# Optimization experiments

Hardware: AMD Instinct MI355X
Metric: run time of the kernel (lower is better)

Reference implementation:

```python
import jax, jax.numpy as jnp
import numpy as np

B, T, D, H = 4, 2048, 1024, 16
HD = D // H  # 64
EPS = 1e-5

def _layernorm(x, g, b):
    mu = jnp.mean(x, axis=-1, keepdims=True)
    var = jnp.var(x, axis=-1, keepdims=True)
    return (x - mu) * jax.lax.rsqrt(var + EPS) * g + b

def setup_inputs() -> dict:
    key = jax.random.key(0)
    ks = jax.random.split(key, 8)
    s = D ** -0.5
    return {
        "x":  jax.random.normal(ks[0], (B, T, D), jnp.float32),
        "Wq": jax.random.normal(ks[1], (H, D, HD), jnp.float32) * s,
        "Wk": jax.random.normal(ks[2], (H, D, HD), jnp.float32) * s,
        "Wv": jax.random.normal(ks[3], (H, D, HD), jnp.float32) * s,
        "Wp": jax.random.normal(ks[4], (D, D), jnp.float32) * s,
        "bp": jnp.zeros((D,), jnp.float32),
        "W1": jax.random.normal(ks[5], (D, 4 * D), jnp.float32) * s,
        "b1": jnp.zeros((4 * D,), jnp.float32),
        "W2": jax.random.normal(ks[6], (4 * D, D), jnp.float32) * (4 * D) ** -0.5,
        "b2": jnp.zeros((D,), jnp.float32),
        "g1": jnp.ones((D,), jnp.float32),
        "be1": jnp.zeros((D,), jnp.float32),
        "g2": jnp.ones((D,), jnp.float32),
        "be2": jnp.zeros((D,), jnp.float32),
    }

def reference(x, Wq, Wk, Wv, Wp, bp, W1, b1, W2, b2, g1, be1, g2, be2):
    # --- pre-LN causal MHA (all heads batched; torch code loops per head) ---
    h = _layernorm(x, g1, be1)                       # [B,T,D]
    q = jnp.einsum('btd,hdk->bhtk', h, Wq)
    k = jnp.einsum('btd,hdk->bhtk', h, Wk)
    v = jnp.einsum('btd,hdk->bhtk', h, Wv)
    scores = jnp.einsum('bhtk,bhsk->bhts', q, k) * (HD ** -0.5)
    causal = jnp.tril(jnp.ones((T, T), bool))
    scores = jnp.where(causal, scores, -jnp.inf)
    w = jax.nn.softmax(scores, axis=-1)              # [B,H,T,T]
    o = jnp.einsum('bhts,bhsk->bhtk', w, v)          # [B,H,T,HD]
    o = o.transpose(0, 2, 1, 3).reshape(x.shape[0], x.shape[1], D)  # concat heads
    x = x + o @ Wp + bp                              # residual 1
    # --- pre-LN FFN ---
    h2 = _layernorm(x, g2, be2)
    ff = jax.nn.relu(h2 @ W1 + b1) @ W2 + b2
    return x + ff
```

## Files before the change

kernel.cpp:

```cpp
#include <hip/hip_runtime.h>
#include <hip/hip_bf16.h>
#include <math.h>

#define Bsz 4
#define Tsz 2048
#define Dsz 1024
#define Hn  16
#define HDs 64

typedef __attribute__((ext_vector_type(8))) short bf16x8;
typedef __attribute__((ext_vector_type(4))) float f32x4;

typedef const __attribute__((address_space(1))) void gvoid;
typedef __attribute__((address_space(3))) void lvoid;

__device__ __forceinline__ void async_copy16(const short* g, short* l) {
    __builtin_amdgcn_global_load_lds((gvoid*)g, (lvoid*)l, 16, 0, 0);
}

__device__ __forceinline__ short f2bf(float x) {
    __hip_bfloat16 h = __float2bfloat16(x);
    return *reinterpret_cast<short*>(&h);
}

__device__ __forceinline__ unsigned int pack_bf16(float hi, float lo) {
    unsigned int uh = __float_as_uint(hi) + 0x8000u;
    unsigned int ul = __float_as_uint(lo) + 0x8000u;
    return __builtin_amdgcn_perm(uh, ul, 0x07060302u);
}

__device__ __forceinline__ size_t headed_idx(int m, int c) {
    int b = m >> 11, t = m & 2047, h = c >> 6, kc = c & 63;
    return (((size_t)(b * Hn + h) * Tsz + t) << 6) + kc;
}

__global__ __launch_bounds__(256) void ln_kernel(const float* __restrict__ x,
                                                 const float* __restrict__ g,
                                                 const float* __restrict__ beta,
                                                 short* __restrict__ out)
{
    const int row = blockIdx.x;
    const float* xr = x + (size_t)row * Dsz;
    float v[4];
    float s = 0.f, s2 = 0.f;
#pragma unroll
    for (int i = 0; i < 4; ++i) {
        v[i] = xr[threadIdx.x + 256 * i];
        s += v[i];
        s2 += v[i] * v[i];
    }
#pragma unroll
    for (int off = 32; off; off >>= 1) {
        s  += __shfl_xor(s,  off);
        s2 += __shfl_xor(s2, off);
    }
    __shared__ float red[8];
    const int wave = threadIdx.x >> 6;
    if ((threadIdx.x & 63) == 0) { red[wave * 2] = s; red[wave * 2 + 1] = s2; }
    __syncthreads();
    s  = red[0] + red[2] + red[4] + red[6];
    s2 = red[1] + red[3] + red[5] + red[7];
    const float mu  = s * (1.f / Dsz);
    const float var = s2 * (1.f / Dsz) - mu * mu;
    const float rs  = rsqrtf(var + 1e-5f);
    short* orow = out + (size_t)row * Dsz;
#pragma unroll
    for (int i = 0; i < 4; ++i) {
        int col = threadIdx.x + 256 * i;
        orow[col] = f2bf((v[i] - mu) * rs * g[col] + beta[col]);
    }
}

__global__ __launch_bounds__(256) void transpose_cvt(
    const float* __restrict__ in, short* __restrict__ outp, int R, int C)
{
    __shared__ float tile[32][33];
    const int r0 = blockIdx.y * 32, c0 = blockIdx.x * 32;
    const size_t so = (size_t)blockIdx.z * R * C;
    const int tx = threadIdx.x & 31, ty = threadIdx.x >> 5;
    const float* ip = in + so;
    short* op = outp + so;
#pragma unroll
    for (int i = 0; i < 4; ++i)
        tile[ty + i * 8][tx] = ip[(size_t)(r0 + ty + i * 8) * C + c0 + tx];
    __syncthreads();
#pragma unroll
    for (int i = 0; i < 4; ++i)
        op[(size_t)(c0 + ty + i * 8) * R + r0 + tx] = f2bf(tile[tx][ty + i * 8]);
}

__global__ __launch_bounds__(256) void transpose_cvt_qkv(
    const float* __restrict__ Wq, const float* __restrict__ Wk,
    const float* __restrict__ Wv, short* __restrict__ outp)
{
    __shared__ float tile[32][33];
    const int z = blockIdx.z;
    const float* in = (z < 16) ? Wq : (z < 32) ? Wk : Wv;
    const int zz = z & 15;
    const int r0 = blockIdx.y * 32, c0 = blockIdx.x * 32;
    const int tx = threadIdx.x & 31, ty = threadIdx.x >> 5;
    const float* ip = in + (size_t)zz * (1024 * 64);
    short* op = outp + (size_t)z * (1024 * 64);
#pragma unroll
    for (int i = 0; i < 4; ++i)
        tile[ty + i * 8][tx] = ip[(size_t)(r0 + ty + i * 8) * 64 + c0 + tx];
    __syncthreads();
#pragma unroll
    for (int i = 0; i < 4; ++i)
        op[(size_t)(c0 + ty + i * 8) * 1024 + r0 + tx] = f2bf(tile[tx][ty + i * 8]);
}

template <int EPI>
__global__ __launch_bounds__(256) void gemm_mfma(
    const short* __restrict__ A, const short* __restrict__ Bt,
    const float* __restrict__ bias, const float* __restrict__ resid,
    float* __restrict__ Cf, short* __restrict__ Cb0,
    short* __restrict__ Cb1, short* __restrict__ Cb2,
    int M, int N, int K, float scale)
{
    __shared__ short As[128 * 32];
    __shared__ short Bs[128 * 32];
    const int tid  = threadIdx.x;
    const int lane = tid & 63, wave = tid >> 6;
    const int quad = lane >> 4, l16 = lane & 15;
    const int m0 = blockIdx.y * 128, n0 = blockIdx.x * 128;
    const int wm = (wave >> 1) * 64, wn = (wave & 1) * 64;

    f32x4 acc[4][4];
#pragma unroll
    for (int i = 0; i < 4; ++i)
#pragma unroll
        for (int j = 0; j < 4; ++j) acc[i][j] = f32x4{0.f, 0.f, 0.f, 0.f};

    const short* gA = A  + (size_t)(m0 + wave * 32 + (lane >> 2)) * K + (lane & 3) * 8;
    const short* gB = Bt + (size_t)(n0 + wave * 32 + (lane >> 2)) * K + (lane & 3) * 8;
    short* lA0 = As + wave * 1024;
    short* lA1 = As + wave * 1024 + 512;
    short* lB0 = Bs + wave * 1024;
    short* lB1 = Bs + wave * 1024 + 512;
    const size_t rstep = (size_t)16 * K;

    for (int k0 = 0; k0 < K; k0 += 32) {
        async_copy16(gA,         lA0);
        async_copy16(gA + rstep, lA1);
        async_copy16(gB,         lB0);
        async_copy16(gB + rstep, lB1);
        gA += 32; gB += 32;
        __syncthreads();
        bf16x8 af[4], bfr[4];
#pragma unroll
        for (int mt = 0; mt < 4; ++mt)
            af[mt] = *(const bf16x8*)(As + (wm + mt * 16 + l16) * 32 + quad * 8);
#pragma unroll
        for (int nt = 0; nt < 4; ++nt)
            bfr[nt] = *(const bf16x8*)(Bs + (wn + nt * 16 + l16) * 32 + quad * 8);
#pragma unroll
        for (int mt = 0; mt < 4; ++mt)
#pragma unroll
            for (int nt = 0; nt < 4; ++nt)
                acc[mt][nt] = __builtin_amdgcn_mfma_f32_16x16x32_bf16(
                    af[mt], bfr[nt], acc[mt][nt], 0, 0, 0);
        __syncthreads();
    }

#pragma unroll
    for (int mt = 0; mt < 4; ++mt) {
#pragma unroll
        for (int nt = 0; nt < 4; ++nt) {
#pragma unroll
            for (int r = 0; r < 4; ++r) {
                const int m = m0 + wm + mt * 16 + quad * 4 + r;
                const int c = n0 + wn + nt * 16 + l16;
                float val = acc[mt][nt][r];
                if (EPI == 0) {
                    const int sel = c >> 10, cl = c & 1023;
                    if (sel == 0)
                        Cb0[headed_idx(m, cl)] = f2bf(val * scale);
                    else if (sel == 1)
                        Cb1[headed_idx(m, cl)] = f2bf(val);
                    else {
                        int b = m >> 11, t = m & 2047;
                        size_t idx = ((((size_t)((b << 4) | (cl >> 6)) << 6) | (cl & 63)) << 11) | t;
                        Cb2[idx] = f2bf(val);
                    }
                } else if (EPI == 2) {
                    size_t idx = (size_t)m * N + c;
                    Cf[idx] = val + bias[c] + resid[idx];
                } else {
                    float v2 = val + bias[c];
                    Cb0[(size_t)m * N + c] = f2bf(v2 > 0.f ? v2 : 0.f);
                }
            }
        }
    }
}

__global__ __launch_bounds__(256, 3) void fattn_kernel(
    const short* __restrict__ Q,
    const short* __restrict__ K,
    const short* __restrict__ VT,
    short* __restrict__ O)
{
    __shared__ short Kl[2][64 * 64];
    __shared__ short Vl[2][64 * 64];
    __shared__ short p_lds[4][2][16 * 64];
    const int tid  = threadIdx.x;
    const int lane = tid & 63, wave = tid >> 6;
    const int quad = lane >> 4, l16 = lane & 15;

    const int tile = 15 - blockIdx.x;
    const int q0   = tile * 128;
    const int q0w  = q0 + wave * 32;
    const int bh   = blockIdx.y;
    const int bb = bh >> 4, hh = bh & 15;
    const size_t bhoff = (size_t)bh * (Tsz * HDs);
    const short* Qb = Q + bhoff;
    const short* Kb = K + bhoff;
    const short* Vb = VT + bhoff;

    const int s_a = tid, s_b = tid + 256;
    const int ra = s_a >> 3, ga = (s_a & 7) ^ (ra & 7);
    const int rb = s_b >> 3, gb = (s_b & 7) ^ (rb & 7);

    short* pw[2] = { &p_lds[wave][0][0], &p_lds[wave][1][0] };
    const int rd0 = l16 * 64 + (((quad    ) ^ (l16 & 7)) << 3);
    const int rd1 = l16 * 64 + (((quad + 4) ^ (l16 & 7)) << 3);

    bf16x8 bq[2][2];
#pragma unroll
    for (int mt = 0; mt < 2; ++mt) {
        const short* qp = Qb + (size_t)(q0w + mt * 16 + l16) * 64 + quad * 8;
        bq[mt][0] = *(const bf16x8*)qp;
        bq[mt][1] = *(const bf16x8*)(qp + 32);
    }

    f32x4 oaccT[2][4];
    float lacc[2] = {0.f, 0.f};
#pragma unroll
    for (int mt = 0; mt < 2; ++mt)
#pragma unroll
        for (int nt = 0; nt < 4; ++nt) oaccT[mt][nt] = f32x4{0.f, 0.f, 0.f, 0.f};

    const int nch  = (q0 + 127) / 64 + 1;
    const int cmax = (q0w + 31) / 64;

    auto stage = [&](int c, int buf) {
        const int c64 = c * 64;
        short* kb_l = &Kl[buf][0];
        short* vb_l = &Vl[buf][0];
        async_copy16(Kb + (((size_t)(c64 + ra)) << 6) + (ga << 3), kb_l + s_a * 8);
        async_copy16(Kb + (((size_t)(c64 + rb)) << 6) + (gb << 3), kb_l + s_b * 8);
        async_copy16(Vb + ((size_t)ra << 11) + c64 + (ga << 3), vb_l + s_a * 8);
        async_copy16(Vb + ((size_t)rb << 11) + c64 + (gb << 3), vb_l + s_b * 8);
    };

    stage(0, 0);
    __syncthreads();

    for (int c = 0; c < nch; ++c) {
        const int cur = c & 1;
        if (c + 1 < nch) stage(c + 1, cur ^ 1);

        if (c <= cmax) {
            const int s0 = c * 64;
            const short* Kc = &Kl[cur][0];
            const short* Vc = &Vl[cur][0];
            bf16x8 ak[4][2], av[4][2];
#pragma unroll
            for (int ct = 0; ct < 4; ++ct) {
                const int r = ct * 16 + l16;
                ak[ct][0] = *(const bf16x8*)(Kc + r * 64 + (((quad    ) ^ (r & 7)) << 3));
                ak[ct][1] = *(const bf16x8*)(Kc + r * 64 + (((quad + 4) ^ (r & 7)) << 3));
            }
#pragma unroll
            for (int nt = 0; nt < 4; ++nt) {
                const int r = nt * 16 + l16;
                av[nt][0] = *(const bf16x8*)(Vc + r * 64 + (((quad    ) ^ (r & 7)) << 3));
                av[nt][1] = *(const bf16x8*)(Vc + r * 64 + (((quad + 4) ^ (r & 7)) << 3));
            }
            f32x4 sfr[2][4];
#pragma unroll
            for (int mt = 0; mt < 2; ++mt)
#pragma unroll
                for (int ct = 0; ct < 4; ++ct) {
                    f32x4 cc = {0.f, 0.f, 0.f, 0.f};
                    cc = __builtin_amdgcn_mfma_f32_16x16x32_bf16(ak[ct][0], bq[mt][0], cc, 0, 0, 0);
                    cc = __builtin_amdgcn_mfma_f32_16x16x32_bf16(ak[ct][1], bq[mt][1], cc, 0, 0, 0);
                    sfr[mt][ct] = cc;
                }
            if (s0 + 63 > q0w) {
#pragma unroll
                for (int mt = 0; mt < 2; ++mt) {
                    const int qr = q0w + mt * 16 + l16;
#pragma unroll
                    for (int ct = 0; ct < 4; ++ct)
#pragma unroll
                        for (int r = 0; r < 4; ++r)
                            if (s0 + ct * 16 + quad * 4 + r > qr)
                                sfr[mt][ct][r] = -INFINITY;
                }
            }
#pragma unroll
            for (int mt = 0; mt < 2; ++mt) {
#pragma unroll
                for (int ct = 0; ct < 4; ++ct) {
                    float p0 = __builtin_exp2f(sfr[mt][ct][0]);
                    float p1 = __builtin_exp2f(sfr[mt][ct][1]);
                    float p2 = __builtin_exp2f(sfr[mt][ct][2]);
                    float p3 = __builtin_exp2f(sfr[mt][ct][3]);
                    lacc[mt] += (p0 + p1) + (p2 + p3);
                    uint2 pkv;
                    pkv.x = pack_bf16(p1, p0);
                    pkv.y = pack_bf16(p3, p2);
                    const int g = (2 * ct + (quad >> 1)) ^ (l16 & 7);
                    *(uint2*)(pw[mt] + l16 * 64 + (g << 3) + (quad & 1) * 4) = pkv;
                }
            }
            bf16x8 bp[2][2];
            bp[0][0] = *(const bf16x8*)(pw[0] + rd0);
            bp[0][1] = *(const bf16x8*)(pw[0] + rd1);
            bp[1][0] = *(const bf16x8*)(pw[1] + rd0);
            bp[1][1] = *(const bf16x8*)(pw[1] + rd1);
#pragma unroll
            for (int nt = 0; nt < 4; ++nt)
#pragma unroll
                for (int mt = 0; mt < 2; ++mt) {
                    oaccT[mt][nt] = __builtin_amdgcn_mfma_f32_16x16x32_bf16(av[nt][0], bp[mt][0], oaccT[mt][nt], 0, 0, 0);
                    oaccT[mt][nt] = __builtin_amdgcn_mfma_f32_16x16x32_bf16(av[nt][1], bp[mt][1], oaccT[mt][nt], 0, 0, 0);
                }
        }
        __syncthreads();
    }

#pragma unroll
    for (int mt = 0; mt < 2; ++mt) {
        float ps = lacc[mt];
        ps += __shfl_xor(ps, 16);
        ps += __shfl_xor(ps, 32);
        const float inv = 1.f / ps;
        short* orow = O + (size_t)(bb * Tsz + q0w + mt * 16 + l16) * Dsz + hh * 64;
#pragma unroll
        for (int nt = 0; nt < 4; ++nt) {
            uint2 pkv;
            pkv.x = pack_bf16(oaccT[mt][nt][1] * inv, oaccT[mt][nt][0] * inv);
            pkv.y = pack_bf16(oaccT[mt][nt][3] * inv, oaccT[mt][nt][2] * inv);
            *(uint2*)(orow + nt * 16 + quad * 4) = pkv;
        }
    }
}

extern "C" void kernel_launch(void* const* d_in, const int* in_sizes, int n_in,
                              void* d_out, int out_size, void* d_ws, size_t ws_size,
                              hipStream_t stream) {
    const float* x   = (const float*)d_in[0];
    const float* Wq  = (const float*)d_in[1];
    const float* Wk  = (const float*)d_in[2];
    const float* Wv  = (const float*)d_in[3];
    const float* Wp  = (const float*)d_in[4];
    const float* bp  = (const float*)d_in[5];
    const float* W1  = (const float*)d_in[6];
    const float* b1  = (const float*)d_in[7];
    const float* W2  = (const float*)d_in[8];
    const float* b2  = (const float*)d_in[9];
    const float* g1  = (const float*)d_in[10];
    const float* be1 = (const float*)d_in[11];
    const float* g2  = (const float*)d_in[12];
    const float* be2 = (const float*)d_in[13];
    float* out = (float*)d_out;
    char*  W   = (char*)d_ws;

    short* h1  = (short*)(W);
    short* ff1 = (short*)(W);
    short* qb  = (short*)(W + (16ull << 20));
    short* kb  = (short*)(W + (32ull << 20));
    short* vtb = (short*)(W + (48ull << 20));
    short* o   = (short*)(W + (64ull << 20));
    short* h2  = (short*)(W + (80ull << 20));
    short* wqt = (short*)(W + (96ull << 20));
    short* wpt = (short*)(W + (102ull << 20));
    short* w1t = (short*)(W + (104ull << 20));
    short* w2t = (short*)(W + (112ull << 20));

    const int M = Bsz * Tsz;
    const float qscale = 0.125f * 1.44269504f;

    transpose_cvt_qkv<<<dim3(2, 32, 48), 256, 0, stream>>>(Wq, Wk, Wv, wqt);
    transpose_cvt<<<dim3(32, 32, 1),  256, 0, stream>>>(Wp, wpt, 1024, 1024);
    transpose_cvt<<<dim3(128, 32, 1), 256, 0, stream>>>(W1, w1t, 1024, 4096);
    transpose_cvt<<<dim3(32, 128, 1), 256, 0, stream>>>(W2, w2t, 4096, 1024);

    ln_kernel<<<dim3(M), 256, 0, stream>>>(x, g1, be1, h1);

    gemm_mfma<0><<<dim3(24, 64), 256, 0, stream>>>(
        h1, wqt, nullptr, nullptr, nullptr, qb, kb, vtb, M, 3072, 1024, qscale);

    fattn_kernel<<<dim3(16, Bsz * Hn), 256, 0, stream>>>(qb, kb, vtb, o);

    gemm_mfma<2><<<dim3(8, 64), 256, 0, stream>>>(
        o, wpt, bp, x, out, nullptr, nullptr, nullptr, M, 1024, 1024, 1.f);

    ln_kernel<<<dim3(M), 256, 0, stream>>>(out, g2, be2, h2);

    gemm_mfma<3><<<dim3(32, 64), 256, 0, stream>>>(
        h2, w1t, b1, nullptr, nullptr, ff1, nullptr, nullptr, M, 4096, 1024, 1.f);

    gemm_mfma<2><<<dim3(8, 64), 256, 0, stream>>>(
        ff1, w2t, b2, out, out, nullptr, nullptr, nullptr, M, 1024, 4096, 1.f);
}
```

Baseline: 596.6 us.

## Pair causal attention tiles per block and remap blocks across XCDs

Each attention block now handles two 64-row query tiles (tile 31-px and tile px), so every block does the same amount of causal work. Block indices are remapped so the heads sharing K/V land on the same XCD, which should improve L2 reuse. Each wave now covers 16 query rows instead of 32, which halves the P scratch in LDS and allows an occupancy hint of 4. The cost is less MFMA work per K/V chunk load, more barriers, and a prefetch chained between the two tiles.

```diff
diff --git a/kernel.cpp b/kernel.cpp
--- a/kernel.cpp
+++ b/kernel.cpp
@@ -195,7 +195,7 @@
     }
 }
 
-__global__ __launch_bounds__(256, 3) void fattn_kernel(
+__global__ __launch_bounds__(256, 4) void fattn_kernel(
     const short* __restrict__ Q,
     const short* __restrict__ K,
     const short* __restrict__ VT,
@@ -203,15 +203,18 @@
 {
     __shared__ short Kl[2][64 * 64];
     __shared__ short Vl[2][64 * 64];
-    __shared__ short p_lds[4][2][16 * 64];
+    __shared__ short p_lds[4][16 * 64];
     const int tid  = threadIdx.x;
     const int lane = tid & 63, wave = tid >> 6;
     const int quad = lane >> 4, l16 = lane & 15;
 
-    const int tile = 15 - blockIdx.x;
-    const int q0   = tile * 128;
-    const int q0w  = q0 + wave * 32;
-    const int bh   = blockIdx.y;
+    const int lin  = blockIdx.y * 16 + blockIdx.x;
+    const int xcd  = lin & 7;
+    const int slot = lin >> 3;
+    const int bh   = xcd * 8 + (slot >> 4);
+    const int px   = slot & 15;
+    const int tiles[2] = { 31 - px, px };
+
     const int bb = bh >> 4, hh = bh & 15;
     const size_t bhoff = (size_t)bh * (Tsz * HDs);
     const short* Qb = Q + bhoff;
@@ -222,30 +225,19 @@
     const int ra = s_a >> 3, ga = (s_a & 7) ^ (ra & 7);
     const int rb = s_b >> 3, gb = (s_b & 7) ^ (rb & 7);
 
-    short* pw[2] = { &p_lds[wave][0][0], &p_lds[wave][1][0] };
+    short* pw = &p_lds[wave][0];
     const int rd0 = l16 * 64 + (((quad    ) ^ (l16 & 7)) << 3);
     const int rd1 = l16 * 64 + (((quad + 4) ^ (l16 & 7)) << 3);
 
     bf16x8 bq[2][2];
 #pragma unroll
-    for (int mt = 0; mt < 2; ++mt) {
-        const short* qp = Qb + (size_t)(q0w + mt * 16 + l16) * 64 + quad * 8;
-        bq[mt][0] = *(const bf16x8*)qp;
-        bq[mt][1] = *(const bf16x8*)(qp + 32);
-    }
-
-    f32x4 oaccT[2][4];
-    float lacc[2] = {0.f, 0.f};
-#pragma unroll
-    for (int mt = 0; mt < 2; ++mt)
-#pragma unroll
-        for (int nt = 0; nt < 4; ++nt) oaccT[mt][nt] = f32x4{0.f, 0.f, 0.f, 0.f};
-
-    const int nch  = (q0 + 127) / 64 + 1;
-    const int cmax = (q0w + 31) / 64;
-
-    auto stage = [&](int c, int buf) {
-        const int c64 = c * 64;
+    for (int ti = 0; ti < 2; ++ti) {
+        const short* qp = Qb + (size_t)(tiles[ti] * 64 + wave * 16 + l16) * 64 + quad * 8;
+        bq[ti][0] = *(const bf16x8*)qp;
+        bq[ti][1] = *(const bf16x8*)(qp + 32);
+    }
+
+    auto stage = [&](int c64, int buf) {
         short* kb_l = &Kl[buf][0];
         short* vb_l = &Vl[buf][0];
         async_copy16(Kb + (((size_t)(c64 + ra)) << 6) + (ga << 3), kb_l + s_a * 8);
@@ -254,14 +246,26 @@
         async_copy16(Vb + ((size_t)rb << 11) + c64 + (gb << 3), vb_l + s_b * 8);
     };
 
-    stage(0, 0);
+    stage(tiles[0] * 0, 0);
     __syncthreads();
 
-    for (int c = 0; c < nch; ++c) {
-        const int cur = c & 1;
-        if (c + 1 < nch) stage(c + 1, cur ^ 1);
-
-        if (c <= cmax) {
+    int phase = 0;
+#pragma unroll
+    for (int ti = 0; ti < 2; ++ti) {
+        const int tile = tiles[ti];
+        const int q0w  = tile * 64 + wave * 16;
+        const int nch  = tile + 1;
+
+        f32x4 oaccT[4];
+        float lacc = 0.f;
+#pragma unroll
+        for (int nt = 0; nt < 4; ++nt) oaccT[nt] = f32x4{0.f, 0.f, 0.f, 0.f};
+
+        for (int c = 0; c < nch; ++c) {
+            const int cur = phase & 1;
+            if (c + 1 < nch)   stage((c + 1) * 64, cur ^ 1);
+            else if (ti == 0)  stage(0, cur ^ 1);
+
             const int s0 = c * 64;
             const short* Kc = &Kl[cur][0];
             const short* Vc = &Vl[cur][0];
@@ -278,72 +282,57 @@
                 av[nt][0] = *(const bf16x8*)(Vc + r * 64 + (((quad    ) ^ (r & 7)) << 3));
                 av[nt][1] = *(const bf16x8*)(Vc + r * 64 + (((quad + 4) ^ (r & 7)) << 3));
             }
-            f32x4 sfr[2][4];
-#pragma unroll
-            for (int mt = 0; mt < 2; ++mt)
-#pragma unroll
-                for (int ct = 0; ct < 4; ++ct) {
-                    f32x4 cc = {0.f, 0.f, 0.f, 0.f};
-                    cc = __builtin_amdgcn_mfma_f32_16x16x32_bf16(ak[ct][0], bq[mt][0], cc, 0, 0, 0);
-                    cc = __builtin_amdgcn_mfma_f32_16x16x32_bf16(ak[ct][1], bq[mt][1], cc, 0, 0, 0);
-                    sfr[mt][ct] = cc;
-                }
+            f32x4 sfr[4];
+#pragma unroll
+            for (int ct = 0; ct < 4; ++ct) {
+                f32x4 cc = {0.f, 0.f, 0.f, 0.f};
+                cc = __builtin_amdgcn_mfma_f32_16x16x32_bf16(ak[ct][0], bq[ti][0], cc, 0, 0, 0);
+                cc = __builtin_amdgcn_mfma_f32_16x16x32_bf16(ak[ct][1], bq[ti][1], cc, 0, 0, 0);
+                sfr[ct] = cc;
+            }
             if (s0 + 63 > q0w) {
-#pragma unroll
-                for (int mt = 0; mt < 2; ++mt) {
-                    const int qr = q0w + mt * 16 + l16;
-#pragma unroll
-                    for (int ct = 0; ct < 4; ++ct)
-#pragma unroll
-                        for (int r = 0; r < 4; ++r)
-                            if (s0 + ct * 16 + quad * 4 + r > qr)
-                                sfr[mt][ct][r] = -INFINITY;
-                }
-            }
-#pragma unroll
-            for (int mt = 0; mt < 2; ++mt) {
-#pragma unroll
-                for (int ct = 0; ct < 4; ++ct) {
-                    float p0 = __builtin_exp2f(sfr[mt][ct][0]);
-                    float p1 = __builtin_exp2f(sfr[mt][ct][1]);
-                    float p2 = __builtin_exp2f(sfr[mt][ct][2]);
-                    float p3 = __builtin_exp2f(sfr[mt][ct][3]);
-                    lacc[mt] += (p0 + p1) + (p2 + p3);
-                    uint2 pkv;
-                    pkv.x = pack_bf16(p1, p0);
-                    pkv.y = pack_bf16(p3, p2);
-                    const int g = (2 * ct + (quad >> 1)) ^ (l16 & 7);
-                    *(uint2*)(pw[mt] + l16 * 64 + (g << 3) + (quad & 1) * 4) = pkv;
-                }
-            }
-            bf16x8 bp[2][2];
-            bp[0][0] = *(const bf16x8*)(pw[0] + rd0);
-            bp[0][1] = *(const bf16x8*)(pw[0] + rd1);
-            bp[1][0] = *(const bf16x8*)(pw[1] + rd0);
-            bp[1][1] = *(const bf16x8*)(pw[1] + rd1);
-#pragma unroll
-            for (int nt = 0; nt < 4; ++nt)
-#pragma unroll
-                for (int mt = 0; mt < 2; ++mt) {
-                    oaccT[mt][nt] = __builtin_amdgcn_mfma_f32_16x16x32_bf16(av[nt][0], bp[mt][0], oaccT[mt][nt], 0, 0, 0);
-                    oaccT[mt][nt] = __builtin_amdgcn_mfma_f32_16x16x32_bf16(av[nt][1], bp[mt][1], oaccT[mt][nt], 0, 0, 0);
-                }
+                const int qr = q0w + l16;
+#pragma unroll
+                for (int ct = 0; ct < 4; ++ct)
+#pragma unroll
+                    for (int r = 0; r < 4; ++r)
+                        if (s0 + ct * 16 + quad * 4 + r > qr)
+                            sfr[ct][r] = -INFINITY;
+            }
+#pragma unroll
+            for (int ct = 0; ct < 4; ++ct) {
+                float p0 = __builtin_exp2f(sfr[ct][0]);
+                float p1 = __builtin_exp2f(sfr[ct][1]);
+                float p2 = __builtin_exp2f(sfr[ct][2]);
+                float p3 = __builtin_exp2f(sfr[ct][3]);
+                lacc += (p0 + p1) + (p2 + p3);
+                uint2 pkv;
+                pkv.x = pack_bf16(p1, p0);
+                pkv.y = pack_bf16(p3, p2);
+                const int g = (2 * ct + (quad >> 1)) ^ (l16 & 7);
+                *(uint2*)(pw + l16 * 64 + (g << 3) + (quad & 1) * 4) = pkv;
+            }
+            bf16x8 bp0 = *(const bf16x8*)(pw + rd0);
+            bf16x8 bp1 = *(const bf16x8*)(pw + rd1);
+#pragma unroll
+            for (int nt = 0; nt < 4; ++nt) {
+                oaccT[nt] = __builtin_amdgcn_mfma_f32_16x16x32_bf16(av[nt][0], bp0, oaccT[nt], 0, 0, 0);
+                oaccT[nt] = __builtin_amdgcn_mfma_f32_16x16x32_bf16(av[nt][1], bp1, oaccT[nt], 0, 0, 0);
+            }
+            __syncthreads();
+            ++phase;
         }
-        __syncthreads();
-    }
-
-#pragma unroll
-    for (int mt = 0; mt < 2; ++mt) {
-        float ps = lacc[mt];
+
+        float ps = lacc;
         ps += __shfl_xor(ps, 16);
         ps += __shfl_xor(ps, 32);
         const float inv = 1.f / ps;
-        short* orow = O + (size_t)(bb * Tsz + q0w + mt * 16 + l16) * Dsz + hh * 64;
+        short* orow = O + (size_t)(bb * Tsz + q0w + l16) * Dsz + hh * 64;
 #pragma unroll
         for (int nt = 0; nt < 4; ++nt) {
             uint2 pkv;
-            pkv.x = pack_bf16(oaccT[mt][nt][1] * inv, oaccT[mt][nt][0] * inv);
-            pkv.y = pack_bf16(oaccT[mt][nt][3] * inv, oaccT[mt][nt][2] * inv);
+            pkv.x = pack_bf16(oaccT[nt][1] * inv, oaccT[nt][0] * inv);
+            pkv.y = pack_bf16(oaccT[nt][3] * inv, oaccT[nt][2] * inv);
             *(uint2*)(orow + nt * 16 + quad * 4) = pkv;
         }
     }
```

Result: faster. 557.5 us (-6.6%).
